# Kernel optimization log

Hardware: AMD Instinct MI355X
Metric: run time of the kernel (lower is better)

Reference implementation:

```python
import jax, jax.numpy as jnp
import numpy as np

N_NODES = 50000
N_EDGES = 800000
IN_DIM = 2
HID = 256
OUT = 16
MLP_H = 256
N_MID = 10  # middle GCN layers (256->256); total 12 layers
EPS = 1e-5


def _bn(x, g, b):
    # BatchNorm1d forward with batch statistics (training-mode math, deterministic)
    m = jnp.mean(x, axis=0)
    v = jnp.var(x, axis=0)
    return (x - m) * jax.lax.rsqrt(v + EPS) * g + b


def _conv(h, W, b, row, col, ew):
    # CutGCNConv: linear transform then edge-weighted scatter-add (source->target)
    h = h @ W + b                      # [N, out]
    msg = ew[:, None] * h[row]         # gather + scale, [E, out]
    return jax.ops.segment_sum(msg, col, num_segments=N_NODES)


def setup_inputs() -> dict:
    key = jax.random.key(0)
    ks = iter(jax.random.split(key, 32))
    d = {}
    d["x"] = jax.random.normal(next(ks), (N_NODES, IN_DIM), dtype=jnp.float32)
    d["edge_index"] = jax.random.randint(next(ks), (2, N_EDGES), 0, N_NODES, dtype=jnp.int32)
    d["edge_weight"] = jax.random.uniform(next(ks), (N_EDGES,), dtype=jnp.float32)
    # GCN params
    d["W0"] = jax.random.normal(next(ks), (IN_DIM, HID), dtype=jnp.float32) / np.sqrt(IN_DIM)
    d["b0"] = jnp.zeros((HID,), jnp.float32)
    d["Wm"] = jax.random.normal(next(ks), (N_MID, HID, HID), dtype=jnp.float32) / np.sqrt(HID)
    d["bm"] = jnp.zeros((N_MID, HID), jnp.float32)
    d["Wl"] = jax.random.normal(next(ks), (HID, OUT), dtype=jnp.float32) / np.sqrt(HID)
    d["bl"] = jnp.zeros((OUT,), jnp.float32)
    # BatchNorms: one before each GCN layer + one after the stack
    d["bn0_g"] = jnp.ones((IN_DIM,), jnp.float32); d["bn0_b"] = jnp.zeros((IN_DIM,), jnp.float32)
    d["bnm_g"] = jnp.ones((N_MID + 1, HID), jnp.float32); d["bnm_b"] = jnp.zeros((N_MID + 1, HID), jnp.float32)
    d["bno_g"] = jnp.ones((OUT,), jnp.float32); d["bno_b"] = jnp.zeros((OUT,), jnp.float32)
    # edge MLP params
    d["mW1"] = jax.random.normal(next(ks), (2 * OUT, MLP_H), dtype=jnp.float32) / np.sqrt(2 * OUT)
    d["mb1"] = jnp.zeros((MLP_H,), jnp.float32)
    d["mbn_g"] = jnp.ones((MLP_H,), jnp.float32); d["mbn_b"] = jnp.zeros((MLP_H,), jnp.float32)
    d["mW2"] = jax.random.normal(next(ks), (MLP_H, 1), dtype=jnp.float32) / np.sqrt(MLP_H)
    d["mb2"] = jnp.zeros((1,), jnp.float32)
    return d


def reference(x, edge_index, edge_weight, W0, b0, Wm, bm, Wl, bl,
              bn0_g, bn0_b, bnm_g, bnm_b, bno_g, bno_b,
              mW1, mb1, mbn_g, mbn_b, mW2, mb2):
    row, col = edge_index[0], edge_index[1]
    # GCN stack (dropout is identity in eval; ReLU after each conv)
    h = jax.nn.relu(_conv(_bn(x, bn0_g, bn0_b), W0, b0, row, col, edge_weight))
    for i in range(N_MID):
        h = jax.nn.relu(_conv(_bn(h, bnm_g[i], bnm_b[i]), Wm[i], bm[i], row, col, edge_weight))
    h = jax.nn.relu(_conv(_bn(h, bnm_g[N_MID], bnm_b[N_MID]), Wl, bl, row, col, edge_weight))
    h = _bn(h, bno_g, bno_b)  # final BatchNorm on gnn_out_dims

    def mlp(e):  # e: [E, 2*OUT]
        z = jax.nn.relu(_bn(e @ mW1 + mb1, mbn_g, mbn_b))
        return (z @ mW2 + mb2)[:, 0]

    hr, hc = h[row], h[col]
    p1 = mlp(jnp.concatenate([hr, hc], axis=1))
    # roll(shifts=16, dims=1) on a 32-wide tensor swaps the halves
    p2 = mlp(jnp.concatenate([hc, hr], axis=1))
    return jax.nn.sigmoid(0.5 * (p1 + p2))
```

## Files before the change

kernel.cpp:

```cpp
#include <hip/hip_runtime.h>
#include <hip/hip_bf16.h>
#include <hip/hip_fp16.h>
#include <math.h>

#define NNODES 50000
#define NEDGES 800000

#define OFF_COUNTS   0ull
#define OFF_DOUT     200704ull
#define OFF_CURSOR   401408ull
#define OFF_WIN      602112ull
#define OFF_STATS2   802816ull
#define OFF_SP8      806912ull
#define OFF_MOM      1167360ull
#define ZERO_END     1218560ull
#define OFF_ST       1218560ull
#define OFF_ABW      1220608ull
#define OFF_OFFSETS  1226752ull
#define OFF_SROW     1427456ull
#define OFF_SEW      4627456ull
#define OFF_TMP16    7827456ull
#define OFF_HRAW     11027456ull
#define OFF_WT       14227456ull
#define OFF_WP       15538176ull
#define OFF_Z        15570944ull
#define OFF_AGGZ     17172480ull
#define OFF_BUFQ     20372480ull
#define OFF_BUFP     45972480ull

typedef __attribute__((ext_vector_type(8))) _Float16 f16x8;
typedef __attribute__((ext_vector_type(4))) float f32x4;

union H4 { ushort4 u; __half h[4]; };
union HU { ushort u; __half h; };

static __device__ inline ushort f2h(float f) {
    HU cv; cv.h = __float2half(f); return cv.u;
}
static __device__ inline float h2f(ushort u) {
    HU cv; cv.u = u; return __half2float(cv.h);
}


__global__ void hist_kernel(const int* __restrict__ ei, const float* __restrict__ ew,
                            int* __restrict__ counts, int* __restrict__ dout,
                            float* __restrict__ w_in, int E) {
    for (int i = blockIdx.x * blockDim.x + threadIdx.x; i < E; i += gridDim.x * blockDim.x) {
        int r = ei[i];
        int c = ei[E + i];
        atomicAdd(&counts[c], 1);
        atomicAdd(&dout[r], 1);
        atomicAdd(&w_in[c], ew[i]);
    }
}

__global__ void scan_kernel(const int* __restrict__ counts, int* __restrict__ offsets, int N) {
    __shared__ int wsum[16];
    __shared__ int carry_s;
    int tid = threadIdx.x;
    int lane = tid & 63, w = tid >> 6;
    if (tid == 0) carry_s = 0;
    __syncthreads();
    for (int base = 0; base < N; base += 1024) {
        int v = (base + tid < N) ? counts[base + tid] : 0;
        int x = v;
#pragma unroll
        for (int off = 1; off < 64; off <<= 1) {
            int y = __shfl_up(x, off);
            if (lane >= off) x += y;
        }
        if (lane == 63) wsum[w] = x;
        __syncthreads();
        if (w == 0 && lane < 16) {
            int s = wsum[lane];
#pragma unroll
            for (int off = 1; off < 16; off <<= 1) {
                int y = __shfl_up(s, off);
                if (lane >= off) s += y;
            }
            wsum[lane] = s;
        }
        __syncthreads();
        int wbase = (w > 0) ? wsum[w - 1] : 0;
        int incl = carry_s + wbase + x;
        if (base + tid < N) offsets[base + tid] = incl - v;
        __syncthreads();
        if (tid == 0) carry_s += wsum[15];
        __syncthreads();
    }
    if (tid == 0) offsets[N] = carry_s;
}

__global__ void scatter_kernel(const int* __restrict__ ei, const float* __restrict__ ew,
                               const int* __restrict__ offsets, int* __restrict__ cursor,
                               int* __restrict__ srow, float* __restrict__ sew, int E) {
    for (int i = blockIdx.x * blockDim.x + threadIdx.x; i < E; i += gridDim.x * blockDim.x) {
        int c = ei[E + i];
        int p = offsets[c] + atomicAdd(&cursor[c], 1);
        srow[p] = ei[i];
        sew[p] = ew[i];
    }
}


__global__ __launch_bounds__(256) void wconv(const float* __restrict__ Wm,
                                             ushort* __restrict__ Wt) {
    __shared__ float tile[32][33];
    int b = blockIdx.x;
    int layer = b >> 6, t = b & 63;
    int tk = (t >> 3) << 5, tn = (t & 7) << 5;
    int tid = threadIdx.x;
    int r = tid >> 5, c = tid & 31;
    const float* W = Wm + layer * 65536;
#pragma unroll
    for (int i = 0; i < 4; i++) tile[r + i * 8][c] = W[(tk + r + i * 8) * 256 + tn + c];
    __syncthreads();
#pragma unroll
    for (int i = 0; i < 4; i++) {
        int n = tn + r + i * 8, k = tk + c;
        Wt[layer * 65536 + n * 256 + k] = f2h(tile[c][r + i * 8]);
    }
}

__global__ void wprep(const float* __restrict__ mW1, ushort* __restrict__ Wp) {
    int tid = threadIdx.x;
    for (int n = tid; n < 512; n += 256) {
        for (int k = 0; k < 32; k++) {
            float v;
            if (n < 256) v = mW1[k * 256 + n];
            else {
                int n2 = n - 256;
                v = (k < 16) ? mW1[(16 + k) * 256 + n2] : mW1[(k - 16) * 256 + n2];
            }
            Wp[n * 32 + k] = f2h(v);
        }
    }
}


__global__ __launch_bounds__(256) void colstats_wr(const float* __restrict__ h,
                                                   float* __restrict__ sums, int C, int M) {
    int gtid = blockIdx.x * blockDim.x + threadIdx.x;
    int lane = threadIdx.x & 63;
    int c = gtid % C;
    int r = gtid / C;
    int stride = (gridDim.x * blockDim.x) / C;
    float s = 0.f, q = 0.f;
    for (; r < M; r += stride) {
        float v = h[r * C + c];
        s += v; q += v * v;
    }
    for (int m = 32; m >= C; m >>= 1) {
        s += __shfl_xor(s, m);
        q += __shfl_xor(q, m);
    }
    if (lane < C) {
        atomicAdd(&sums[c], s);
        atomicAdd(&sums[C + c], q);
    }
}

__global__ void bn_finalize(const float* __restrict__ sums, const float* __restrict__ g,
                            const float* __restrict__ b, float* __restrict__ st, int C, int M) {
    int c = threadIdx.x;
    if (c >= C) return;
    float mean = sums[c] / (float)M;
    float var  = sums[C + c] / (float)M - mean * mean;
    float sc = g[c] * rsqrtf(var + 1e-5f);
    st[c] = sc;
    st[C + c] = b[c] - mean * sc;
}

__global__ void bn_finalize16(const float* __restrict__ sp, const float* __restrict__ g,
                              const float* __restrict__ b, float* __restrict__ st, int M) {
    int c = threadIdx.x;
    float s = 0.f, q = 0.f;
#pragma unroll
    for (int p = 0; p < 16; p++) { s += sp[p * 512 + c]; q += sp[p * 512 + 256 + c]; }
    float mean = s / (float)M;
    float var  = q / (float)M - mean * mean;
    float sc = g[c] * rsqrtf(var + 1e-5f);
    st[c] = sc;
    st[256 + c] = b[c] - mean * sc;
}


__global__ __launch_bounds__(256) void gemm_mfma(const __half* __restrict__ H,
                                                 const ushort* __restrict__ Wt,
                                                 const float* __restrict__ bias,
                                                 const float* __restrict__ sp,
                                                 const float* __restrict__ g,
                                                 const float* __restrict__ b,
                                                 __half* __restrict__ out, int M) {
    __shared__ __attribute__((aligned(16))) ushort Ah[128][40];
    __shared__ __attribute__((aligned(16))) ushort Bh[128][40];
    __shared__ __attribute__((aligned(16))) float st_s[512];
    int tid = threadIdx.x;
    int wid = tid >> 6, lane = tid & 63;
    int m0 = blockIdx.x * 128;
    int n0 = blockIdx.y * 128;
    const ushort* Hu = (const ushort*)H;

    {
        float s = 0.f, q = 0.f;
#pragma unroll
        for (int p = 0; p < 16; p++) { s += sp[p * 512 + tid]; q += sp[p * 512 + 256 + tid]; }
        float invM = 1.f / (float)M;
        float mean = s * invM;
        float var  = q * invM - mean * mean;
        float sc = g[tid] * rsqrtf(var + 1e-5f);
        st_s[tid] = sc;
        st_s[256 + tid] = b[tid] - mean * sc;
    }
    __syncthreads();

    f32x4 acc[2][8];
#pragma unroll
    for (int m = 0; m < 2; m++)
#pragma unroll
        for (int n = 0; n < 8; n++) acc[m][n] = (f32x4){0.f, 0.f, 0.f, 0.f};

    int sr = tid >> 3;
    int kq = (tid & 7) << 2;
    int fr = lane & 15;
    int qo = (lane >> 4) << 3;
    int mrow = wid << 5;

    for (int k0 = 0; k0 < 256; k0 += 32) {
#pragma unroll
        for (int t = 0; t < 4; t++) {
            int r = sr + t * 32;
            int gr = m0 + r; if (gr >= M) gr = M - 1;
            H4 h4; h4.u = *(const ushort4*)(Hu + gr * 256 + k0 + kq);
            float4 s4 = *(const float4*)(st_s + k0 + kq);
            float4 t4 = *(const float4*)(st_s + 256 + k0 + kq);
            ushort4 vh;
            vh.x = f2h(__half2float(h4.h[0]) * s4.x + t4.x);
            vh.y = f2h(__half2float(h4.h[1]) * s4.y + t4.y);
            vh.z = f2h(__half2float(h4.h[2]) * s4.z + t4.z);
            vh.w = f2h(__half2float(h4.h[3]) * s4.w + t4.w);
            *(ushort4*)&Ah[r][kq] = vh;
            ushort4 bh = *(const ushort4*)(Wt + (n0 + r) * 256 + k0 + kq);
            *(ushort4*)&Bh[r][kq] = bh;
        }
        __syncthreads();

        f16x8 a0 = *(const f16x8*)&Ah[mrow + fr][qo];
        f16x8 a1 = *(const f16x8*)&Ah[mrow + 16 + fr][qo];
#pragma unroll
        for (int nt = 0; nt < 8; nt++) {
            f16x8 bb = *(const f16x8*)&Bh[nt * 16 + fr][qo];
            acc[0][nt] = __builtin_amdgcn_mfma_f32_16x16x32_f16(a0, bb, acc[0][nt], 0, 0, 0);
            acc[1][nt] = __builtin_amdgcn_mfma_f32_16x16x32_f16(a1, bb, acc[1][nt], 0, 0, 0);
        }
        __syncthreads();
    }

#pragma unroll
    for (int mt = 0; mt < 2; mt++) {
        int gmb = m0 + mrow + mt * 16 + ((lane >> 4) << 2);
#pragma unroll
        for (int nt = 0; nt < 8; nt++) {
            int gn = n0 + nt * 16 + fr;
            float bv = bias[gn];
#pragma unroll
            for (int j = 0; j < 4; j++) {
                int gm = gmb + j;
                if (gm < M) out[gm * 256 + gn] = __float2half(acc[mt][nt][j] + bv);
            }
        }
    }
}


__global__ __launch_bounds__(256) void spmm_f16s(const __half* __restrict__ T,
                                                 const int* __restrict__ srow,
                                                 const float* __restrict__ sew,
                                                 const int* __restrict__ off,
                                                 __half* __restrict__ outp,
                                                 float* __restrict__ sp, int N) {
    __shared__ float red[4][512];
    int tid = threadIdx.x;
    int wid = tid >> 6, lane = tid & 63;
    int l4 = lane << 2;
    int gw = blockIdx.x * 4 + wid, nw = gridDim.x * 4;
    const ushort* Tu = (const ushort*)T;
    ushort* Ou = (ushort*)outp;
    float cs[4] = {0, 0, 0, 0}, cq[4] = {0, 0, 0, 0};
    for (int n = gw; n < N; n += nw) {
        int e0 = off[n], e1 = off[n + 1];
        float4 acc = {0.f, 0.f, 0.f, 0.f};
        int e = e0;
        for (; e + 7 < e1; e += 8) {
            int r[8]; float w[8]; H4 v[8];
#pragma unroll
            for (int i = 0; i < 8; i++) { r[i] = srow[e + i]; w[i] = sew[e + i]; }
#pragma unroll
            for (int i = 0; i < 8; i++) v[i].u = *(const ushort4*)(Tu + r[i] * 256 + l4);
#pragma unroll
            for (int i = 0; i < 8; i++) {
                acc.x += w[i] * __half2float(v[i].h[0]);
                acc.y += w[i] * __half2float(v[i].h[1]);
                acc.z += w[i] * __half2float(v[i].h[2]);
                acc.w += w[i] * __half2float(v[i].h[3]);
            }
        }
        for (; e < e1; ++e) {
            int rr = srow[e]; float w = sew[e];
            H4 v; v.u = *(const ushort4*)(Tu + rr * 256 + l4);
            acc.x += w * __half2float(v.h[0]);
            acc.y += w * __half2float(v.h[1]);
            acc.z += w * __half2float(v.h[2]);
            acc.w += w * __half2float(v.h[3]);
        }
        acc.x = fmaxf(acc.x, 0.f); acc.y = fmaxf(acc.y, 0.f);
        acc.z = fmaxf(acc.z, 0.f); acc.w = fmaxf(acc.w, 0.f);
        H4 o;
        o.h[0] = __float2half(acc.x); o.h[1] = __float2half(acc.y);
        o.h[2] = __float2half(acc.z); o.h[3] = __float2half(acc.w);
        *(ushort4*)(Ou + n * 256 + l4) = o.u;
        cs[0] += acc.x; cq[0] += acc.x * acc.x;
        cs[1] += acc.y; cq[1] += acc.y * acc.y;
        cs[2] += acc.z; cq[2] += acc.z * acc.z;
        cs[3] += acc.w; cq[3] += acc.w * acc.w;
    }
#pragma unroll
    for (int j = 0; j < 4; j++) {
        red[wid][l4 + j] = cs[j];
        red[wid][256 + l4 + j] = cq[j];
    }
    __syncthreads();
    float* dst = sp + (blockIdx.x & 15) * 512;
    for (int i = tid; i < 512; i += 256)
        atomicAdd(&dst[i], red[0][i] + red[1][i] + red[2][i] + red[3][i]);
}

__global__ __launch_bounds__(256) void spmm_small(const float* __restrict__ T,
                                                  const int* __restrict__ srow,
                                                  const float* __restrict__ sew,
                                                  const int* __restrict__ off,
                                                  float* __restrict__ out,
                                                  int C, int N, int relu) {
    int npb = blockDim.x / C;
    int local = threadIdx.x / C;
    int c = threadIdx.x % C;
    int n = blockIdx.x * npb + local;
    if (n >= N) return;
    int e0 = off[n], e1 = off[n + 1];
    float acc = 0.f;
    for (int e = e0; e < e1; ++e) acc += sew[e] * T[srow[e] * C + c];
    if (relu) acc = fmaxf(acc, 0.f);
    out[n * C + c] = acc;
}


__global__ __launch_bounds__(256) void layer0_fin(const float* __restrict__ agg2,
                                                  const float* __restrict__ w_in,
                                                  const float* __restrict__ st,
                                                  const float* __restrict__ W0,
                                                  const float* __restrict__ b0,
                                                  __half* __restrict__ h,
                                                  float* __restrict__ sp, int N) {
    int j = threadIdx.x;
    float w0j = W0[j], w1j = W0[256 + j], b0j = b0[j];
    float s0 = st[0], s1 = st[1], t0 = st[2], t1 = st[3];
    float cs = 0.f, cq = 0.f;
    for (int n = blockIdx.x; n < N; n += gridDim.x) {
        float wi = w_in[n];
        float a0 = agg2[n * 2 + 0] * s0 + wi * t0;
        float a1 = agg2[n * 2 + 1] * s1 + wi * t1;
        float v = fmaxf(a0 * w0j + a1 * w1j + wi * b0j, 0.f);
        h[n * 256 + j] = __float2half(v);
        cs += v; cq += v * v;
    }
    float* dst = sp + (blockIdx.x & 15) * 512;
    atomicAdd(&dst[j], cs);
    atomicAdd(&dst[256 + j], cq);
}


__global__ __launch_bounds__(256) void gemm16(const __half* __restrict__ H,
                                              const float* __restrict__ Wl,
                                              const float* __restrict__ bl,
                                              const float* __restrict__ st,
                                              float* __restrict__ out, int M) {
    __shared__ float Hs[16][256];
    __shared__ float Ws[256][16];
    int tid = threadIdx.x;
    int n0 = blockIdx.x << 4;
    const ushort* Hu = (const ushort*)H;
    for (int i = tid; i < 4096; i += 256) Ws[i >> 4][i & 15] = Wl[i];
    for (int i = tid; i < 4096; i += 256) {
        int r = i >> 8, k = i & 255;
        int n = n0 + r;
        float hv = 0.f;
        if (n < M) hv = h2f(Hu[n * 256 + k]) * st[k] + st[256 + k];
        Hs[r][k] = hv;
    }
    __syncthreads();
    int r = tid >> 4, j = tid & 15;
    float acc = bl[j];
    for (int k = 0; k < 256; k++) acc += Hs[r][k] * Ws[k][j];
    if (n0 + r < M) out[(n0 + r) * 16 + j] = acc;
}


__global__ void zprep(const float* __restrict__ hraw, const float* __restrict__ st,
                      ushort* __restrict__ Z, int NE) {
    int i = blockIdx.x * blockDim.x + threadIdx.x;
    if (i >= NE) return;
    int c = i & 15;
    Z[i] = f2h(hraw[i] * st[c] + st[16 + c]);
}


__global__ __launch_bounds__(256) void aggz_spmm(const ushort* __restrict__ Z,
                                                 const int* __restrict__ srow,
                                                 const int* __restrict__ off,
                                                 float* __restrict__ aggz, int N) {
    int local = threadIdx.x >> 4;
    int c = threadIdx.x & 15;
    int n = blockIdx.x * 16 + local;
    if (n >= N) return;
    int e0 = off[n], e1 = off[n + 1];
    float acc = 0.f;
    for (int e = e0; e < e1; ++e) acc += h2f(Z[srow[e] * 16 + c]);
    aggz[n * 16 + c] = acc;
}


__global__ __launch_bounds__(256) void zmom(const ushort* __restrict__ Z,
                                            const float* __restrict__ aggz,
                                            const int* __restrict__ dout,
                                            const int* __restrict__ din,
                                            float* __restrict__ MOM, int N) {
    __shared__ float zs[128][17];
    __shared__ float az[128][17];
    __shared__ float dw[128][2];
    int tid = threadIdx.x;
    int i = tid >> 4, j = tid & 15;
    float p = 0.f, r = 0.f, m = 0.f, sdo = 0.f, sdi = 0.f;
    for (int base = blockIdx.x * 128; base < N; base += gridDim.x * 128) {
        int cnt = N - base; if (cnt > 128) cnt = 128;
        for (int t = tid; t < 2048; t += 256) {
            int n = t >> 4, c = t & 15;
            if (n < cnt) {
                zs[n][c] = h2f(Z[(base + n) * 16 + c]);
                az[n][c] = aggz[(base + n) * 16 + c];
            } else { zs[n][c] = 0.f; az[n][c] = 0.f; }
        }
        for (int t = tid; t < 128; t += 256) {
            if (t < cnt) { dw[t][0] = (float)dout[base + t]; dw[t][1] = (float)din[base + t]; }
            else { dw[t][0] = 0.f; dw[t][1] = 0.f; }
        }
        __syncthreads();
        for (int n = 0; n < 128; n++) {
            float zi = zs[n][i], zj = zs[n][j];
            float d0 = dw[n][0], d1 = dw[n][1];
            float zz = zi * zj;
            p += d0 * zz;
            r += d1 * zz;
            m += az[n][i] * zj;
            if (i == 0) { sdo += d0 * zj; sdi += d1 * zj; }
        }
        __syncthreads();
    }
    float* dst = MOM + (blockIdx.x & 15) * 800;
    atomicAdd(&dst[tid], p);
    atomicAdd(&dst[256 + tid], r);
    atomicAdd(&dst[512 + tid], m);
    if (i == 0) { atomicAdd(&dst[768 + j], sdo); atomicAdd(&dst[784 + j], sdi); }
}


__global__ __launch_bounds__(256) void mlp_ab(const float* __restrict__ MOM,
                                              const float* __restrict__ mW1,
                                              const float* __restrict__ g,
                                              const float* __restrict__ b,
                                              const float* __restrict__ mW2,
                                              float* __restrict__ abw, int E) {
    __shared__ float P[256], R[256], Mm[256], Sdo[16], Sdi[16];
    int tid = threadIdx.x;
    float sp = 0.f, sr = 0.f, sm = 0.f;
#pragma unroll
    for (int q = 0; q < 16; q++) {
        sp += MOM[q * 800 + tid];
        sr += MOM[q * 800 + 256 + tid];
        sm += MOM[q * 800 + 512 + tid];
    }
    P[tid] = sp; R[tid] = sr; Mm[tid] = sm;
    if (tid < 16) {
        float a = 0.f, c = 0.f;
#pragma unroll
        for (int q = 0; q < 16; q++) { a += MOM[q * 800 + 768 + tid]; c += MOM[q * 800 + 784 + tid]; }
        Sdo[tid] = a; Sdi[tid] = c;
    }
    __syncthreads();
    int j = tid;
    float A[16], B[16];
#pragma unroll
    for (int k = 0; k < 16; k++) { A[k] = mW1[k * 256 + j]; B[k] = mW1[(16 + k) * 256 + j]; }
    float apa = 0.f, brb = 0.f, amb = 0.f, bpb = 0.f, ara = 0.f, bma = 0.f;
    float aso = 0.f, bso = 0.f, asi = 0.f, bsi = 0.f;
    for (int i2 = 0; i2 < 16; i2++) {
        float Ai = A[i2], Bi = B[i2];
        aso += Ai * Sdo[i2]; bso += Bi * Sdo[i2];
        asi += Ai * Sdi[i2]; bsi += Bi * Sdi[i2];
#pragma unroll
        for (int k = 0; k < 16; k++) {
            float Pik = P[i2 * 16 + k], Rik = R[i2 * 16 + k], Mik = Mm[i2 * 16 + k];
            apa += Ai * Pik * A[k]; brb += Bi * Rik * B[k]; amb += Ai * Mik * B[k];
            bpb += Bi * Pik * B[k]; ara += Ai * Rik * A[k]; bma += Bi * Mik * A[k];
        }
    }
    float invE = 1.f / (float)E;
    float mu1 = (aso + bsi) * invE;
    float mu2 = (bso + asi) * invE;
    float e21 = (apa + brb + 2.f * amb) * invE;
    float e22 = (bpb + ara + 2.f * bma) * invE;
    float v1 = e21 - mu1 * mu1;
    float v2 = e22 - mu2 * mu2;
    float a1 = g[j] * rsqrtf(v1 + 1e-5f);
    float a2 = g[j] * rsqrtf(v2 + 1e-5f);
    abw[j] = a1;                 abw[256 + j] = a2;
    abw[512 + j] = b[j] - mu1 * a1; abw[768 + j] = b[j] - mu2 * a2;
    abw[1024 + j] = mW2[j];      abw[1280 + j] = mW2[j];
}


__global__ __launch_bounds__(256) void edge_mfma(const ushort* __restrict__ Z,
                                                 const int* __restrict__ ei,
                                                 const ushort* __restrict__ Wp,
                                                 const float* __restrict__ abw,
                                                 const float* __restrict__ mb2,
                                                 float* __restrict__ out, int E) {
    __shared__ __attribute__((aligned(16))) ushort As[256][40];
    __shared__ __attribute__((aligned(16))) ushort Bs[512][40];
    int tid = threadIdx.x;
    int wid = tid >> 6, lane = tid & 63;
    int fr = lane & 15, qo = (lane >> 4) << 3;

    for (int i = tid * 4; i < 512 * 32; i += 1024) {
        int n = i >> 5, k = i & 31;
        *(ushort4*)&Bs[n][k] = *(const ushort4*)(Wp + i);
    }
    int e0 = blockIdx.x * 256;
    {
        int e = e0 + tid;
        int r = 0, c = 0;
        if (e < E) { r = ei[e]; c = ei[E + e]; }
        uint4 z0 = *(const uint4*)(Z + r * 16);
        uint4 z1 = *(const uint4*)(Z + r * 16 + 8);
        uint4 z2 = *(const uint4*)(Z + c * 16);
        uint4 z3 = *(const uint4*)(Z + c * 16 + 8);
        *(uint4*)&As[tid][0]  = z0; *(uint4*)&As[tid][8]  = z1;
        *(uint4*)&As[tid][16] = z2; *(uint4*)&As[tid][24] = z3;
    }
    __syncthreads();

    f16x8 a[4];
#pragma unroll
    for (int mt = 0; mt < 4; mt++) a[mt] = *(const f16x8*)&As[(wid * 4 + mt) * 16 + fr][qo];
    float pacc[4][4];
#pragma unroll
    for (int mt = 0; mt < 4; mt++)
#pragma unroll
        for (int j = 0; j < 4; j++) pacc[mt][j] = 0.f;
    float mb2v = mb2[0];

    for (int n = 0; n < 32; n++) {
        f16x8 bfr = *(const f16x8*)&Bs[n * 16 + fr][qo];
        int col = n * 16 + fr;
        float av = abw[col], bv = abw[512 + col], wv = abw[1024 + col];
#pragma unroll
        for (int mt = 0; mt < 4; mt++) {
            f32x4 c0 = {0.f, 0.f, 0.f, 0.f};
            c0 = __builtin_amdgcn_mfma_f32_16x16x32_f16(a[mt], bfr, c0, 0, 0, 0);
#pragma unroll
            for (int j = 0; j < 4; j++)
                pacc[mt][j] += fmaxf(c0[j] * av + bv, 0.f) * wv;
        }
    }

#pragma unroll
    for (int mt = 0; mt < 4; mt++)
#pragma unroll
        for (int j = 0; j < 4; j++) {
            float p = pacc[mt][j];
            p += __shfl_xor(p, 1);
            p += __shfl_xor(p, 2);
            p += __shfl_xor(p, 4);
            p += __shfl_xor(p, 8);
            if (fr == 0) {
                int row = (wid * 4 + mt) * 16 + ((lane >> 4) << 2) + j;
                int e = e0 + row;
                if (e < E) out[e] = 1.f / (1.f + expf(-(0.5f * p + mb2v)));
            }
        }
}


extern "C" void kernel_launch(void* const* d_in, const int* in_sizes, int n_in,
                              void* d_out, int out_size, void* d_ws, size_t ws_size,
                              hipStream_t stream) {
    const float* x     = (const float*)d_in[0];
    const int*   ei    = (const int*)d_in[1];
    const float* ew    = (const float*)d_in[2];
    const float* W0    = (const float*)d_in[3];
    const float* b0    = (const float*)d_in[4];
    const float* Wm    = (const float*)d_in[5];
    const float* bm    = (const float*)d_in[6];
    const float* Wl    = (const float*)d_in[7];
    const float* bl    = (const float*)d_in[8];
    const float* bn0_g = (const float*)d_in[9];
    const float* bn0_b = (const float*)d_in[10];
    const float* bnm_g = (const float*)d_in[11];
    const float* bnm_b = (const float*)d_in[12];
    const float* bno_g = (const float*)d_in[13];
    const float* bno_b = (const float*)d_in[14];
    const float* mW1   = (const float*)d_in[15];
    const float* mbn_g = (const float*)d_in[17];
    const float* mbn_b = (const float*)d_in[18];
    const float* mW2   = (const float*)d_in[19];
    const float* mb2   = (const float*)d_in[20];
    float* outp = (float*)d_out;

    char* ws = (char*)d_ws;
    int*    counts  = (int*)(ws + OFF_COUNTS);
    int*    dout    = (int*)(ws + OFF_DOUT);
    int*    cursor  = (int*)(ws + OFF_CURSOR);
    float*  w_in    = (float*)(ws + OFF_WIN);
    float*  stats2  = (float*)(ws + OFF_STATS2);
    float*  sp8     = (float*)(ws + OFF_SP8);
    float*  MOM     = (float*)(ws + OFF_MOM);
    float*  st      = (float*)(ws + OFF_ST);
    float*  abw     = (float*)(ws + OFF_ABW);
    int*    offsets = (int*)(ws + OFF_OFFSETS);
    int*    srow    = (int*)(ws + OFF_SROW);
    float*  sew     = (float*)(ws + OFF_SEW);
    float*  tmp16   = (float*)(ws + OFF_TMP16);
    float*  hraw    = (float*)(ws + OFF_HRAW);
    ushort* Wt      = (ushort*)(ws + OFF_WT);
    ushort* Wp      = (ushort*)(ws + OFF_WP);
    ushort* Z       = (ushort*)(ws + OFF_Z);
    float*  aggz    = (float*)(ws + OFF_AGGZ);
    __half* bufQ    = (__half*)(ws + OFF_BUFQ);
    __half* bufP    = (__half*)(ws + OFF_BUFP);
    float*  agg2    = tmp16;

    const int N = NNODES, E = NEDGES;

    hipMemsetAsync(ws, 0, ZERO_END, stream);

    hist_kernel<<<1024, 256, 0, stream>>>(ei, ew, counts, dout, w_in, E);
    wconv<<<640, 256, 0, stream>>>(Wm, Wt);
    wprep<<<1, 256, 0, stream>>>(mW1, Wp);
    scan_kernel<<<1, 1024, 0, stream>>>(counts, offsets, N);
    scatter_kernel<<<1024, 256, 0, stream>>>(ei, ew, offsets, cursor, srow, sew, E);

    colstats_wr<<<64, 256, 0, stream>>>(x, stats2 + 0 * 512, 2, N);
    bn_finalize<<<1, 256, 0, stream>>>(stats2 + 0 * 512, bn0_g, bn0_b, st, 2, N);
    spmm_small<<<(N + 127) / 128, 256, 0, stream>>>(x, srow, sew, offsets, agg2, 2, N, 0);
    layer0_fin<<<512, 256, 0, stream>>>(agg2, w_in, st, W0, b0, bufP, sp8 + 0 * 8192, N);

    for (int i = 0; i < 10; i++) {
        gemm_mfma<<<dim3((N + 127) / 128, 2), 256, 0, stream>>>(
            bufP, Wt + i * 65536, bm + i * 256,
            sp8 + i * 8192, bnm_g + i * 256, bnm_b + i * 256, bufQ, N);
        spmm_f16s<<<2048, 256, 0, stream>>>(bufQ, srow, sew, offsets, bufP,
                                            sp8 + (i + 1) * 8192, N);
    }

    bn_finalize16<<<1, 256, 0, stream>>>(sp8 + 10 * 8192, bnm_g + 10 * 256,
                                         bnm_b + 10 * 256, st, N);
    gemm16<<<(N + 15) / 16, 256, 0, stream>>>(bufP, Wl, bl, st, tmp16, N);
    spmm_small<<<(N + 15) / 16, 256, 0, stream>>>(tmp16, srow, sew, offsets, hraw, 16, N, 1);

    colstats_wr<<<64, 256, 0, stream>>>(hraw, stats2 + 1 * 512, 16, N);
    bn_finalize<<<1, 256, 0, stream>>>(stats2 + 1 * 512, bno_g, bno_b, st, 16, N);
    zprep<<<(N * 16 + 255) / 256, 256, 0, stream>>>(hraw, st, Z, N * 16);

    aggz_spmm<<<(N + 15) / 16, 256, 0, stream>>>(Z, srow, offsets, aggz, N);
    zmom<<<256, 256, 0, stream>>>(Z, aggz, dout, counts, MOM, N);
    mlp_ab<<<1, 256, 0, stream>>>(MOM, mW1, mbn_g, mbn_b, mW2, abw, E);

    edge_mfma<<<(E + 255) / 256, 256, 0, stream>>>(Z, ei, Wp, abw, mb2, outp, E);
}
```

Baseline: 1.691 ms.

## Widen SpMM gathers to 16B with half-wave edge split; pack count+weight atomics

The 256-wide SpMM now has each half-wavefront handle alternate edges, with every lane loading 8 halves (16B) per row, and the two halves are combined by a cross-lane shuffle. The goal is fewer, wider gather instructions and more edges in flight per wave. Separately, the histogram packs the edge count and a fixed-point weight sum into a single 64-bit atomic and records each edge's rank, so the scatter pass needs no second atomic cursor. Workspace buffers are aliased into bufQ to shrink the footprint, and w_in is now accumulated in fixed point, which adds quantization error.

New measurement: 1.544 ms. 1.09x faster.

```diff
diff --git a/kernel.cpp b/kernel.cpp
--- a/kernel.cpp
+++ b/kernel.cpp
@@ -6,32 +6,33 @@
 #define NNODES 50000
 #define NEDGES 800000
 
-#define OFF_COUNTS   0ull
-#define OFF_DOUT     200704ull
-#define OFF_CURSOR   401408ull
-#define OFF_WIN      602112ull
-#define OFF_STATS2   802816ull
-#define OFF_SP8      806912ull
-#define OFF_MOM      1167360ull
-#define ZERO_END     1218560ull
-#define OFF_ST       1218560ull
-#define OFF_ABW      1220608ull
+#define OFF_CW       0ull
+#define OFF_DOUT     401408ull
+#define OFF_STATS2   602112ull
+#define OFF_SP8      606208ull
+#define OFF_MOM      966656ull
+#define ZERO_END     1017856ull
+#define OFF_ST       1017856ull
+#define OFF_ABW      1019904ull
+#define OFF_WIN      1026048ull
 #define OFF_OFFSETS  1226752ull
 #define OFF_SROW     1427456ull
 #define OFF_SEW      4627456ull
-#define OFF_TMP16    7827456ull
-#define OFF_HRAW     11027456ull
-#define OFF_WT       14227456ull
-#define OFF_WP       15538176ull
-#define OFF_Z        15570944ull
-#define OFF_AGGZ     17172480ull
-#define OFF_BUFQ     20372480ull
-#define OFF_BUFP     45972480ull
+#define OFF_RANK     7827456ull
+#define OFF_WT       11027456ull
+#define OFF_WP       12338176ull
+#define OFF_BUFQ     12371968ull
+#define OFF_BUFP     37971968ull
+#define ALI_TMP16    0ull
+#define ALI_HRAW     3276800ull
+#define ALI_Z        6553600ull
+#define ALI_AGGZ     8388608ull
 
 typedef __attribute__((ext_vector_type(8))) _Float16 f16x8;
 typedef __attribute__((ext_vector_type(4))) float f32x4;
 
 union H4 { ushort4 u; __half h[4]; };
+union US8 { uint4 u; __half h[8]; };
 union HU { ushort u; __half h; };
 
 static __device__ inline ushort f2h(float f) {
@@ -43,18 +44,21 @@
 
 
 __global__ void hist_kernel(const int* __restrict__ ei, const float* __restrict__ ew,
-                            int* __restrict__ counts, int* __restrict__ dout,
-                            float* __restrict__ w_in, int E) {
+                            unsigned long long* __restrict__ cw, int* __restrict__ dout,
+                            int* __restrict__ rank, int E) {
     for (int i = blockIdx.x * blockDim.x + threadIdx.x; i < E; i += gridDim.x * blockDim.x) {
         int r = ei[i];
         int c = ei[E + i];
-        atomicAdd(&counts[c], 1);
+        unsigned long long pack = (1ull << 40) |
+            (unsigned long long)__float2uint_rn(ew[i] * 1048576.f);
+        unsigned long long old = atomicAdd(&cw[c], pack);
+        rank[i] = (int)(old >> 40);
         atomicAdd(&dout[r], 1);
-        atomicAdd(&w_in[c], ew[i]);
-    }
-}
-
-__global__ void scan_kernel(const int* __restrict__ counts, int* __restrict__ offsets, int N) {
+    }
+}
+
+__global__ void scan_kernel(const unsigned long long* __restrict__ cw,
+                            int* __restrict__ offsets, float* __restrict__ w_in, int N) {
     __shared__ int wsum[16];
     __shared__ int carry_s;
     int tid = threadIdx.x;
@@ -62,7 +66,12 @@
     if (tid == 0) carry_s = 0;
     __syncthreads();
     for (int base = 0; base < N; base += 1024) {
-        int v = (base + tid < N) ? counts[base + tid] : 0;
+        int v = 0;
+        if (base + tid < N) {
+            unsigned long long cv = cw[base + tid];
+            v = (int)(cv >> 40);
+            w_in[base + tid] = (float)(cv & 0xFFFFFFFFFFull) * (1.f / 1048576.f);
+        }
         int x = v;
 #pragma unroll
         for (int off = 1; off < 64; off <<= 1) {
@@ -92,11 +101,11 @@
 }
 
 __global__ void scatter_kernel(const int* __restrict__ ei, const float* __restrict__ ew,
-                               const int* __restrict__ offsets, int* __restrict__ cursor,
+                               const int* __restrict__ offsets, const int* __restrict__ rank,
                                int* __restrict__ srow, float* __restrict__ sew, int E) {
     for (int i = blockIdx.x * blockDim.x + threadIdx.x; i < E; i += gridDim.x * blockDim.x) {
         int c = ei[E + i];
-        int p = offsets[c] + atomicAdd(&cursor[c], 1);
+        int p = offsets[c] + rank[i];
         srow[p] = ei[i];
         sew[p] = ew[i];
     }
@@ -273,7 +282,7 @@
 }
 
 
-__global__ __launch_bounds__(256) void spmm_f16s(const __half* __restrict__ T,
+__global__ __launch_bounds__(256) void spmm_f16w(const __half* __restrict__ T,
                                                  const int* __restrict__ srow,
                                                  const float* __restrict__ sew,
                                                  const int* __restrict__ off,
@@ -282,52 +291,52 @@
     __shared__ float red[4][512];
     int tid = threadIdx.x;
     int wid = tid >> 6, lane = tid & 63;
-    int l4 = lane << 2;
-    int gw = blockIdx.x * 4 + wid, nw = gridDim.x * 4;
+    int hh = lane >> 5;
+    int li = lane & 31;
+    int colb = li << 3;
     const ushort* Tu = (const ushort*)T;
     ushort* Ou = (ushort*)outp;
-    float cs[4] = {0, 0, 0, 0}, cq[4] = {0, 0, 0, 0};
+    float cs[8] = {0, 0, 0, 0, 0, 0, 0, 0}, cq[8] = {0, 0, 0, 0, 0, 0, 0, 0};
+    int gw = blockIdx.x * 4 + wid, nw = gridDim.x * 4;
     for (int n = gw; n < N; n += nw) {
         int e0 = off[n], e1 = off[n + 1];
-        float4 acc = {0.f, 0.f, 0.f, 0.f};
+        float acc[8] = {0, 0, 0, 0, 0, 0, 0, 0};
         int e = e0;
         for (; e + 7 < e1; e += 8) {
-            int r[8]; float w[8]; H4 v[8];
-#pragma unroll
-            for (int i = 0; i < 8; i++) { r[i] = srow[e + i]; w[i] = sew[e + i]; }
-#pragma unroll
-            for (int i = 0; i < 8; i++) v[i].u = *(const ushort4*)(Tu + r[i] * 256 + l4);
-#pragma unroll
-            for (int i = 0; i < 8; i++) {
-                acc.x += w[i] * __half2float(v[i].h[0]);
-                acc.y += w[i] * __half2float(v[i].h[1]);
-                acc.z += w[i] * __half2float(v[i].h[2]);
-                acc.w += w[i] * __half2float(v[i].h[3]);
+            int rr[4]; float wv[4]; US8 v[4];
+#pragma unroll
+            for (int i = 0; i < 4; i++) { rr[i] = srow[e + 2 * i + hh]; wv[i] = sew[e + 2 * i + hh]; }
+#pragma unroll
+            for (int i = 0; i < 4; i++) v[i].u = *(const uint4*)(Tu + rr[i] * 256 + colb);
+#pragma unroll
+            for (int i = 0; i < 4; i++)
+#pragma unroll
+                for (int j = 0; j < 8; j++) acc[j] += wv[i] * __half2float(v[i].h[j]);
+        }
+        for (; e < e1; e += 2) {
+            if (e + hh < e1) {
+                int r = srow[e + hh]; float w = sew[e + hh];
+                US8 v; v.u = *(const uint4*)(Tu + r * 256 + colb);
+#pragma unroll
+                for (int j = 0; j < 8; j++) acc[j] += w * __half2float(v.h[j]);
             }
         }
-        for (; e < e1; ++e) {
-            int rr = srow[e]; float w = sew[e];
-            H4 v; v.u = *(const ushort4*)(Tu + rr * 256 + l4);
-            acc.x += w * __half2float(v.h[0]);
-            acc.y += w * __half2float(v.h[1]);
-            acc.z += w * __half2float(v.h[2]);
-            acc.w += w * __half2float(v.h[3]);
-        }
-        acc.x = fmaxf(acc.x, 0.f); acc.y = fmaxf(acc.y, 0.f);
-        acc.z = fmaxf(acc.z, 0.f); acc.w = fmaxf(acc.w, 0.f);
-        H4 o;
-        o.h[0] = __float2half(acc.x); o.h[1] = __float2half(acc.y);
-        o.h[2] = __float2half(acc.z); o.h[3] = __float2half(acc.w);
-        *(ushort4*)(Ou + n * 256 + l4) = o.u;
-        cs[0] += acc.x; cq[0] += acc.x * acc.x;
-        cs[1] += acc.y; cq[1] += acc.y * acc.y;
-        cs[2] += acc.z; cq[2] += acc.z * acc.z;
-        cs[3] += acc.w; cq[3] += acc.w * acc.w;
-    }
-#pragma unroll
-    for (int j = 0; j < 4; j++) {
-        red[wid][l4 + j] = cs[j];
-        red[wid][256 + l4 + j] = cq[j];
+        US8 o;
+#pragma unroll
+        for (int j = 0; j < 8; j++) {
+            float other = __shfl(acc[j], lane ^ 32, 64);
+            float s = fmaxf(acc[j] + other, 0.f);
+            o.h[j] = __float2half(s);
+            if (hh == 0) { cs[j] += s; cq[j] += s * s; }
+        }
+        if (hh == 0) *(uint4*)(Ou + n * 256 + colb) = o.u;
+    }
+    if (hh == 0) {
+#pragma unroll
+        for (int j = 0; j < 8; j++) {
+            red[wid][colb + j] = cs[j];
+            red[wid][256 + colb + j] = cq[j];
+        }
     }
     __syncthreads();
     float* dst = sp + (blockIdx.x & 15) * 512;
@@ -432,7 +441,7 @@
 __global__ __launch_bounds__(256) void zmom(const ushort* __restrict__ Z,
                                             const float* __restrict__ aggz,
                                             const int* __restrict__ dout,
-                                            const int* __restrict__ din,
+                                            const unsigned long long* __restrict__ cw,
                                             float* __restrict__ MOM, int N) {
     __shared__ float zs[128][17];
     __shared__ float az[128][17];
@@ -450,8 +459,10 @@
             } else { zs[n][c] = 0.f; az[n][c] = 0.f; }
         }
         for (int t = tid; t < 128; t += 256) {
-            if (t < cnt) { dw[t][0] = (float)dout[base + t]; dw[t][1] = (float)din[base + t]; }
-            else { dw[t][0] = 0.f; dw[t][1] = 0.f; }
+            if (t < cnt) {
+                dw[t][0] = (float)dout[base + t];
+                dw[t][1] = (float)(int)(cw[base + t] >> 40);
+            } else { dw[t][0] = 0.f; dw[t][1] = 0.f; }
         }
         __syncthreads();
         for (int n = 0; n < 128; n++) {
@@ -626,37 +637,37 @@
     float* outp = (float*)d_out;
 
     char* ws = (char*)d_ws;
-    int*    counts  = (int*)(ws + OFF_COUNTS);
+    unsigned long long* cw = (unsigned long long*)(ws + OFF_CW);
     int*    dout    = (int*)(ws + OFF_DOUT);
-    int*    cursor  = (int*)(ws + OFF_CURSOR);
-    float*  w_in    = (float*)(ws + OFF_WIN);
     float*  stats2  = (float*)(ws + OFF_STATS2);
     float*  sp8     = (float*)(ws + OFF_SP8);
     float*  MOM     = (float*)(ws + OFF_MOM);
     float*  st      = (float*)(ws + OFF_ST);
     float*  abw     = (float*)(ws + OFF_ABW);
+    float*  w_in    = (float*)(ws + OFF_WIN);
     int*    offsets = (int*)(ws + OFF_OFFSETS);
     int*    srow    = (int*)(ws + OFF_SROW);
     float*  sew     = (float*)(ws + OFF_SEW);
-    float*  tmp16   = (float*)(ws + OFF_TMP16);
-    float*  hraw    = (float*)(ws + OFF_HRAW);
+    int*    rank    = (int*)(ws + OFF_RANK);
     ushort* Wt      = (ushort*)(ws + OFF_WT);
     ushort* Wp      = (ushort*)(ws + OFF_WP);
-    ushort* Z       = (ushort*)(ws + OFF_Z);
-    float*  aggz    = (float*)(ws + OFF_AGGZ);
     __half* bufQ    = (__half*)(ws + OFF_BUFQ);
     __half* bufP    = (__half*)(ws + OFF_BUFP);
-    float*  agg2    = tmp16;
+    float*  agg2    = (float*)(ws + OFF_BUFQ + ALI_TMP16);
+    float*  tmp16   = (float*)(ws + OFF_BUFQ + ALI_TMP16);
+    float*  hraw    = (float*)(ws + OFF_BUFQ + ALI_HRAW);
+    ushort* Z       = (ushort*)(ws + OFF_BUFQ + ALI_Z);
+    float*  aggz    = (float*)(ws + OFF_BUFQ + ALI_AGGZ);
 
     const int N = NNODES, E = NEDGES;
 
     hipMemsetAsync(ws, 0, ZERO_END, stream);
 
-    hist_kernel<<<1024, 256, 0, stream>>>(ei, ew, counts, dout, w_in, E);
+    hist_kernel<<<1024, 256, 0, stream>>>(ei, ew, cw, dout, rank, E);
     wconv<<<640, 256, 0, stream>>>(Wm, Wt);
     wprep<<<1, 256, 0, stream>>>(mW1, Wp);
-    scan_kernel<<<1, 1024, 0, stream>>>(counts, offsets, N);
-    scatter_kernel<<<1024, 256, 0, stream>>>(ei, ew, offsets, cursor, srow, sew, E);
+    scan_kernel<<<1, 1024, 0, stream>>>(cw, offsets, w_in, N);
+    scatter_kernel<<<1024, 256, 0, stream>>>(ei, ew, offsets, rank, srow, sew, E);
 
     colstats_wr<<<64, 256, 0, stream>>>(x, stats2 + 0 * 512, 2, N);
     bn_finalize<<<1, 256, 0, stream>>>(stats2 + 0 * 512, bn0_g, bn0_b, st, 2, N);
@@ -667,7 +678,7 @@
         gemm_mfma<<<dim3((N + 127) / 128, 2), 256, 0, stream>>>(
             bufP, Wt + i * 65536, bm + i * 256,
             sp8 + i * 8192, bnm_g + i * 256, bnm_b + i * 256, bufQ, N);
-        spmm_f16s<<<2048, 256, 0, stream>>>(bufQ, srow, sew, offsets, bufP,
+        spmm_f16w<<<2048, 256, 0, stream>>>(bufQ, srow, sew, offsets, bufP,
                                             sp8 + (i + 1) * 8192, N);
     }
 
@@ -681,7 +692,7 @@
     zprep<<<(N * 16 + 255) / 256, 256, 0, stream>>>(hraw, st, Z, N * 16);
 
     aggz_spmm<<<(N + 15) / 16, 256, 0, stream>>>(Z, srow, offsets, aggz, N);
-    zmom<<<256, 256, 0, stream>>>(Z, aggz, dout, counts, MOM, N);
+    zmom<<<256, 256, 0, stream>>>(Z, aggz, dout, cw, MOM, N);
     mlp_ab<<<1, 256, 0, stream>>>(MOM, mW1, mbn_g, mbn_b, mW2, abw, E);
 
     edge_mfma<<<(E + 255) / 256, 256, 0, stream>>>(Z, ei, Wp, abw, mb2, outp, E);
```
